# Kernel tuning notes

Hardware: AMD Instinct MI355X
Metric: run time of the kernel (lower is better)

## Reference

```python
import jax, jax.numpy as jnp
import numpy as np
import math

HEAD_SIZE = 64
WHERE_CONST = -10000.0


def setup_inputs() -> dict:
    key = jax.random.key(0)
    k1, k2, k3 = jax.random.split(key, 3)
    shape = (4, 16, 2048, 64)  # [B, H, S, D]
    q = jax.random.normal(k1, shape, dtype=jnp.float32)
    k = jax.random.normal(k2, shape, dtype=jnp.float32)
    v = jax.random.normal(k3, shape, dtype=jnp.float32)
    return {"q": q, "k": k, "v": v}


def reference(q, k, v):
    # scores: [B, H, Sq, Sk]
    scale = 1.0 / math.sqrt(HEAD_SIZE)
    scores = jnp.einsum('bhqd,bhkd->bhqk', q, k) * scale
    q_len, k_len = q.shape[-2], k.shape[-2]
    causal_mask = jnp.tril(jnp.ones((q_len, k_len), dtype=bool))[None, None]
    scores = jnp.where(causal_mask, scores, WHERE_CONST)
    probs = jax.nn.softmax(scores, axis=-1)
    # dropout rate is 0.0 -> identity
    out = jnp.einsum('bhqk,bhkd->bhqd', probs, v)  # [B, H, S, D]
    out = jnp.swapaxes(out, 1, 2)                  # [B, S, H, D]
    B, S, H, D = out.shape
    return out.reshape(B, S, H * D)
```

## Files before the change

kernel.cpp:

```cpp
#include <hip/hip_runtime.h>
#include <hip/hip_bf16.h>

typedef __bf16 bf16x8_t __attribute__((ext_vector_type(8)));
typedef float  f32x4_t  __attribute__((ext_vector_type(4)));
typedef short  short8_t __attribute__((ext_vector_type(8)));
typedef short  short4_t __attribute__((ext_vector_type(4)));

#define NB   4
#define NH   16
#define SEQ  2048
#define HD   64
#define BQ   128
#define BKV  64
#define LSTR 72

#define MASK2 (-14426.950408889634f)
#define QSCL  (0.18033688011112042f)

__device__ __forceinline__ int swz(int rowi, int blk) {
    return rowi * LSTR + (((blk) ^ (rowi >> 3)) & 7) * 8;
}

__global__ void __launch_bounds__(256)
fa_fwd(const float* __restrict__ qg,
       const float* __restrict__ kg,
       const float* __restrict__ vg,
       float* __restrict__ outg) {
    __shared__ alignas(16) short k_lds[BKV * LSTR];
    __shared__ alignas(16) short vt_lds[HD * LSTR];
    __shared__ alignas(16) short p_lds[BQ * LSTR];

    const int tid  = threadIdx.x;
    const int wave = tid >> 6;
    const int lane = tid & 63;
    const int l16  = lane & 15;
    const int quad = lane >> 4;

    const int bh = blockIdx.x;
    const int qb = (int)gridDim.y - 1 - (int)blockIdx.y;
    const int q0 = qb * BQ;

    const size_t base = (size_t)bh * SEQ * HD;
    const float* qp = qg + base;
    const float* kp = kg + base;
    const float* vp = vg + base;

    bf16x8_t qfA0, qfA1, qfB0, qfB1;
    auto load_q = [&](int row, bf16x8_t& f0, bf16x8_t& f1) {
        const float* qr = qp + (size_t)row * HD;
        f32x4_t a0 = *(const f32x4_t*)(qr + quad * 8);
        f32x4_t a1 = *(const f32x4_t*)(qr + quad * 8 + 4);
        f32x4_t a2 = *(const f32x4_t*)(qr + 32 + quad * 8);
        f32x4_t a3 = *(const f32x4_t*)(qr + 32 + quad * 8 + 4);
        #pragma unroll
        for (int j = 0; j < 4; ++j) {
            f0[j]     = (__bf16)(a0[j] * QSCL);
            f0[4 + j] = (__bf16)(a1[j] * QSCL);
            f1[j]     = (__bf16)(a2[j] * QSCL);
            f1[4 + j] = (__bf16)(a3[j] * QSCL);
        }
    };
    load_q(q0 + wave * 16 + l16, qfA0, qfA1);
    load_q(q0 + 64 + wave * 16 + l16, qfB0, qfB1);

    f32x4_t oA[4], oB[4];
    const f32x4_t zero4 = {0.0f, 0.0f, 0.0f, 0.0f};
    #pragma unroll
    for (int c = 0; c < 4; ++c) { oA[c] = zero4; oB[c] = zero4; }
    float mA = MASK2, lA = 0.0f, mB = MASK2, lB = 0.0f;

    const int sr = tid >> 4;
    const int cb = tid & 15;
    const int d0 = cb * 4;

    f32x4_t kreg[4], vreg[4];

    auto issue = [&](int kt0) {
        const float* kr = kp + (size_t)(kt0 + 4 * sr) * HD + d0;
        const float* vr = vp + (size_t)(kt0 + 4 * sr) * HD + d0;
        #pragma unroll
        for (int i = 0; i < 4; ++i) {
            kreg[i] = *(const f32x4_t*)(kr + i * HD);
            vreg[i] = *(const f32x4_t*)(vr + i * HD);
        }
    };

    auto stage = [&]() {
        #pragma unroll
        for (int i = 0; i < 4; ++i) {
            const int r0 = 4 * sr + i;
            short4_t kw;
            #pragma unroll
            for (int j = 0; j < 4; ++j) kw[j] = __builtin_bit_cast(short, (__bf16)kreg[i][j]);
            *(short4_t*)&k_lds[swz(r0, cb >> 1) + (cb & 1) * 4] = kw;
        }
        #pragma unroll
        for (int j = 0; j < 4; ++j) {
            short4_t vw;
            #pragma unroll
            for (int i = 0; i < 4; ++i) vw[i] = __builtin_bit_cast(short, (__bf16)vreg[i][j]);
            *(short4_t*)&vt_lds[swz(d0 + j, sr >> 1) + (sr & 1) * 4] = vw;
        }
    };

    const int qloc = wave * 16 + l16;

    auto softmax_pstore = [&](const f32x4_t (&s)[4], float& m, float& l,
                              f32x4_t (&o)[4], bool diag, int prow_) {
        float sv[4][4];
        float vmax = MASK2;
        #pragma unroll
        for (int c = 0; c < 4; ++c) {
            #pragma unroll
            for (int r = 0; r < 4; ++r) {
                float x = s[c][r];
                if (diag && (c * 16 + quad * 4 + r > qloc)) x = MASK2;
                sv[c][r] = x;
                vmax = fmaxf(vmax, x);
            }
        }
        vmax = fmaxf(vmax, __shfl_xor(vmax, 16));
        vmax = fmaxf(vmax, __shfl_xor(vmax, 32));
        if (__any((int)(vmax > m))) {
            float mn = fmaxf(m, vmax);
            float a  = __builtin_amdgcn_exp2f(m - mn);
            m = mn;
            l *= a;
            float ar[4];
            #pragma unroll
            for (int r = 0; r < 4; ++r)
                ar[r] = __shfl(a, (lane & 48) | (quad * 4 + r));
            #pragma unroll
            for (int c = 0; c < 4; ++c)
                #pragma unroll
                for (int r = 0; r < 4; ++r)
                    o[c][r] *= ar[r];
        }
        float rs = 0.0f;
        #pragma unroll
        for (int c = 0; c < 4; ++c) {
            short4_t pw;
            #pragma unroll
            for (int r = 0; r < 4; ++r) {
                float p = __builtin_amdgcn_exp2f(sv[c][r] - m);
                rs += p;
                pw[r] = __builtin_bit_cast(short, (__bf16)p);
            }
            *(short4_t*)&p_lds[swz(prow_, 2 * c + (quad >> 1)) + (quad & 1) * 4] = pw;
        }
        rs += __shfl_xor(rs, 16);
        rs += __shfl_xor(rs, 32);
        l += rs;
    };

    issue(0);

    const int ntiles = 2 * qb + 2;
    for (int t = 0; t < ntiles; ++t) {
        const int kt0 = t * BKV;
        __syncthreads();
        stage();
        __syncthreads();
        if (t + 1 < ntiles) issue(kt0 + BKV);

        const bool doA   = (t < ntiles - 1);
        const bool diagA = (t == ntiles - 2);
        const bool diagB = (t == ntiles - 1);

        f32x4_t sA[4], sB[4];
        #pragma unroll
        for (int c = 0; c < 4; ++c) { sA[c] = zero4; sB[c] = zero4; }
        __builtin_amdgcn_s_setprio(1);
        #pragma unroll
        for (int c = 0; c < 4; ++c) {
            const int kvrow = c * 16 + l16;
            bf16x8_t kf0 = __builtin_bit_cast(bf16x8_t, *(const short8_t*)&k_lds[swz(kvrow, quad)]);
            bf16x8_t kf1 = __builtin_bit_cast(bf16x8_t, *(const short8_t*)&k_lds[swz(kvrow, quad + 4)]);
            if (doA) {
                sA[c] = __builtin_amdgcn_mfma_f32_16x16x32_bf16(kf0, qfA0, sA[c], 0, 0, 0);
                sA[c] = __builtin_amdgcn_mfma_f32_16x16x32_bf16(kf1, qfA1, sA[c], 0, 0, 0);
            }
            sB[c] = __builtin_amdgcn_mfma_f32_16x16x32_bf16(kf0, qfB0, sB[c], 0, 0, 0);
            sB[c] = __builtin_amdgcn_mfma_f32_16x16x32_bf16(kf1, qfB1, sB[c], 0, 0, 0);
        }
        __builtin_amdgcn_s_setprio(0);

        const int prowA = wave * 16 + l16;
        if (doA) softmax_pstore(sA, mA, lA, oA, diagA, prowA);
        softmax_pstore(sB, mB, lB, oB, diagB, 64 + prowA);


        bf16x8_t pfA0, pfA1;
        if (doA) {
            pfA0 = __builtin_bit_cast(bf16x8_t, *(const short8_t*)&p_lds[swz(prowA, quad)]);
            pfA1 = __builtin_bit_cast(bf16x8_t, *(const short8_t*)&p_lds[swz(prowA, quad + 4)]);
        }
        bf16x8_t pfB0 = __builtin_bit_cast(bf16x8_t, *(const short8_t*)&p_lds[swz(64 + prowA, quad)]);
        bf16x8_t pfB1 = __builtin_bit_cast(bf16x8_t, *(const short8_t*)&p_lds[swz(64 + prowA, quad + 4)]);
        __builtin_amdgcn_s_setprio(1);
        #pragma unroll
        for (int c = 0; c < 4; ++c) {
            const int d = c * 16 + l16;
            bf16x8_t b0 = __builtin_bit_cast(bf16x8_t, *(const short8_t*)&vt_lds[swz(d, quad)]);
            bf16x8_t b1 = __builtin_bit_cast(bf16x8_t, *(const short8_t*)&vt_lds[swz(d, quad + 4)]);
            if (doA) {
                oA[c] = __builtin_amdgcn_mfma_f32_16x16x32_bf16(pfA0, b0, oA[c], 0, 0, 0);
                oA[c] = __builtin_amdgcn_mfma_f32_16x16x32_bf16(pfA1, b1, oA[c], 0, 0, 0);
            }
            oB[c] = __builtin_amdgcn_mfma_f32_16x16x32_bf16(pfB0, b0, oB[c], 0, 0, 0);
            oB[c] = __builtin_amdgcn_mfma_f32_16x16x32_bf16(pfB1, b1, oB[c], 0, 0, 0);
        }
        __builtin_amdgcn_s_setprio(0);
    }

    const int b = bh >> 4;
    const int h = bh & 15;
    auto store_o = [&](const f32x4_t (&o)[4], float l, int row_base) {
        #pragma unroll
        for (int r = 0; r < 4; ++r) {
            const float lr = __shfl(l, (lane & 48) | (quad * 4 + r));
            const float inv_l = 1.0f / fmaxf(lr, 1e-30f);
            const int row = row_base + quad * 4 + r;
            float* op = outg + ((size_t)b * SEQ + row) * (NH * HD) + h * HD;
            #pragma unroll
            for (int c = 0; c < 4; ++c) {
                float val = o[c][r] * inv_l;
                unsigned bits = __builtin_bit_cast(unsigned, val);
                if ((bits & 0x7F800000u) == 0x7F800000u) val = 0.0f;
                op[c * 16 + l16] = val;
            }
        }
    };
    store_o(oA, lA, q0 + wave * 16);
    store_o(oB, lB, q0 + 64 + wave * 16);
}

extern "C" void kernel_launch(void* const* d_in, const int* in_sizes, int n_in,
                              void* d_out, int out_size, void* d_ws, size_t ws_size,
                              hipStream_t stream) {
    const float* q = (const float*)d_in[0];
    const float* k = (const float*)d_in[1];
    const float* v = (const float*)d_in[2];
    float* out = (float*)d_out;
    dim3 grid(NB * NH, SEQ / BQ);
    fa_fwd<<<grid, 256, 0, stream>>>(q, k, v, out);
}
```

Before: 199.3 us.

## Pair short and long causal query tiles per block to balance work

```diff
diff --git a/kernel.cpp b/kernel.cpp
--- a/kernel.cpp
+++ b/kernel.cpp
@@ -10,8 +10,9 @@
 #define NH   16
 #define SEQ  2048
 #define HD   64
-#define BQ   128
+#define QT   64
 #define BKV  64
+#define NQT  (SEQ / QT)
 #define LSTR 72
 
 #define MASK2 (-14426.950408889634f)
@@ -28,7 +29,7 @@
        float* __restrict__ outg) {
     __shared__ alignas(16) short k_lds[BKV * LSTR];
     __shared__ alignas(16) short vt_lds[HD * LSTR];
-    __shared__ alignas(16) short p_lds[BQ * LSTR];
+    __shared__ alignas(16) short p_lds[2 * QT * LSTR];
 
     const int tid  = threadIdx.x;
     const int wave = tid >> 6;
@@ -37,8 +38,13 @@
     const int quad = lane >> 4;
 
     const int bh = blockIdx.x;
-    const int qb = (int)gridDim.y - 1 - (int)blockIdx.y;
-    const int q0 = qb * BQ;
+    const int pi = blockIdx.y;
+    const int qtA = pi;
+    const int qtB = (NQT - 1) - pi;
+    const int q0A = qtA * QT;
+    const int q0B = qtB * QT;
+    const int ntA = qtA + 1;
+    const int ntB = qtB + 1;
 
     const size_t base = (size_t)bh * SEQ * HD;
     const float* qp = qg + base;
@@ -60,8 +66,8 @@
             f1[4 + j] = (__bf16)(a3[j] * QSCL);
         }
     };
-    load_q(q0 + wave * 16 + l16, qfA0, qfA1);
-    load_q(q0 + 64 + wave * 16 + l16, qfB0, qfB1);
+    load_q(q0A + wave * 16 + l16, qfA0, qfA1);
+    load_q(q0B + wave * 16 + l16, qfB0, qfB1);
 
     f32x4_t oA[4], oB[4];
     const f32x4_t zero4 = {0.0f, 0.0f, 0.0f, 0.0f};
@@ -155,17 +161,16 @@
 
     issue(0);
 
-    const int ntiles = 2 * qb + 2;
-    for (int t = 0; t < ntiles; ++t) {
+    for (int t = 0; t < ntB; ++t) {
         const int kt0 = t * BKV;
         __syncthreads();
         stage();
         __syncthreads();
-        if (t + 1 < ntiles) issue(kt0 + BKV);
-
-        const bool doA   = (t < ntiles - 1);
-        const bool diagA = (t == ntiles - 2);
-        const bool diagB = (t == ntiles - 1);
+        if (t + 1 < ntB) issue(kt0 + BKV);
+
+        const bool doA   = (t < ntA);
+        const bool diagA = (t == ntA - 1);
+        const bool diagB = (t == ntB - 1);
 
         f32x4_t sA[4], sB[4];
         #pragma unroll
@@ -231,8 +236,8 @@
             }
         }
     };
-    store_o(oA, lA, q0 + wave * 16);
-    store_o(oB, lB, q0 + 64 + wave * 16);
+    store_o(oA, lA, q0A + wave * 16);
+    store_o(oB, lB, q0B + wave * 16);
 }
 
 extern "C" void kernel_launch(void* const* d_in, const int* in_sizes, int n_in,
@@ -242,6 +247,6 @@
     const float* k = (const float*)d_in[1];
     const float* v = (const float*)d_in[2];
     float* out = (float*)d_out;
-    dim3 grid(NB * NH, SEQ / BQ);
+    dim3 grid(NB * NH, NQT / 2);
     fa_fwd<<<grid, 256, 0, stream>>>(q, k, v, out);
 }
```

Result: slower. 259.7 us (+30.3%).
